# Optimization experiments

Measured on AMD Instinct MI355X. Metric: run time of the kernel, lower is better.

The kernel has to match this reference:

```python
import jax, jax.numpy as jnp
import numpy as np

B, D, N, C = 8192, 128, 64, 256

def setup_inputs() -> dict:
    key = jax.random.key(0)
    ks = jax.random.split(key, 7)
    s1 = 1.0 / np.sqrt(D)
    s2 = 1.0 / np.sqrt(C)
    return {
        "X": jax.random.normal(ks[0], (B, D, N), dtype=jnp.float32),
        "W1": jax.random.normal(ks[1], (D, C), dtype=jnp.float32) * s1,
        "b1": jax.random.normal(ks[2], (C,), dtype=jnp.float32) * s1,
        "W2": jax.random.normal(ks[3], (C, C), dtype=jnp.float32) * s2,
        "b2": jax.random.normal(ks[4], (C,), dtype=jnp.float32) * s2,
        "W3": jax.random.normal(ks[5], (C, 1), dtype=jnp.float32) * s2,
        "b3": jax.random.normal(ks[6], (1,), dtype=jnp.float32) * s2,
    }

def reference(X, W1, b1, W2, b2, W3, b3):
    # X: (B, D, N); each per-node slice X[:, :, i] goes through the shared MLP.
    # Batched over nodes: one GEMM instead of N tiny launches.
    h = jax.nn.relu(jnp.einsum('bdn,dc->bnc', X, W1) + b1)   # (B, N, C)
    h = jax.nn.relu(jnp.einsum('bnc,ce->bne', h, W2) + b2)   # (B, N, C)
    logits = jnp.einsum('bnc,co->bno', h, W3) + b3           # (B, N, 1)
    logits = logits[..., 0]                                   # (B, N)
    zeros = jnp.zeros((X.shape[0], 1), dtype=logits.dtype)    # add_zero=True
    return jnp.concatenate([zeros, logits], axis=1)           # (B, N+1)
```

## Files before the change

kernel.cpp:

```cpp
#include <hip/hip_runtime.h>
#include <hip/hip_bf16.h>

typedef unsigned short u16;
typedef unsigned int   u32;
typedef __attribute__((ext_vector_type(8))) short bf16x8;
typedef __attribute__((ext_vector_type(4))) float f32x4;

#define NB 8192

__device__ __forceinline__ u32 pack2bf(float a, float b) {
    __hip_bfloat162 h = __float22bfloat162_rn(make_float2(a, b));
    return *reinterpret_cast<u32*>(&h);
}

__device__ __forceinline__ u16 f2bf(float x) {
    u32 u = __float_as_uint(x);
    u32 r = u + 0x7FFFu + ((u >> 16) & 1u);
    return (u16)(r >> 16);
}

__global__ __launch_bounds__(256) void prep_weights(
    const float* __restrict__ W1, const float* __restrict__ W2,
    u16* __restrict__ w1fr, u16* __restrict__ w2fr)
{
    int tid = blockIdx.x * 256 + threadIdx.x;
    if (tid < 32768) {
        const int f = tid >> 9, r = tid & 511, l = r >> 3, j = r & 7;
        const int wv = f >> 4, mt = (f >> 2) & 3, ks = f & 3;
        const int c = 64 * wv + 16 * mt + (l & 15);
        const int d = 32 * ks + 8 * (l >> 4) + j;
        w1fr[tid] = f2bf(W1[d * 256 + c]);
    } else {
        const int t2 = tid - 32768;
        if (t2 < 65536) {
            const int f = t2 >> 9, r = t2 & 511, l = r >> 3, j = r & 7;
            const int wv = f >> 5, et = (f >> 3) & 3, ks = f & 7;
            const int e = 64 * wv + 16 * et + (l & 15);
            const int c = 32 * ks + 8 * (l >> 4) + j;
            w2fr[t2] = f2bf(W2[c * 256 + e]);
        }
    }
}

__global__ __launch_bounds__(256, 4) void fused_mlp(
    const float* __restrict__ X,
    const float* __restrict__ b1, const float* __restrict__ b2,
    const float* __restrict__ W3, const float* __restrict__ b3,
    const u16* __restrict__ w1fr, const u16* __restrict__ w2fr,
    float* __restrict__ out)
{
    __shared__ __align__(16) u16 smem[64 * 256];
    u16* xt   = smem;
    u16* h1s  = smem;
    __shared__ float partl[4][64];

    const int tid = threadIdx.x;
    const int w   = tid >> 6;
    const int l   = tid & 63;
    const int lc  = l & 15;
    const int lk  = l >> 4;
    const int b   = blockIdx.x;
    const float* Xb = X + (size_t)b * 8192;

    const u16* w1b = w1fr + w * 8192  + l * 8;
    const u16* w2b = w2fr + w * 16384 + l * 8;

    #pragma unroll
    for (int it = 0; it < 4; ++it) {
        const int dc = w + 4 * it, d0 = dc << 3;
        float v[8];
        #pragma unroll
        for (int j = 0; j < 8; ++j) v[j] = Xb[(d0 + j) * 64 + l];
        u32 pk[4];
        #pragma unroll
        for (int j = 0; j < 4; ++j) pk[j] = pack2bf(v[2 * j], v[2 * j + 1]);
        *(uint4*)(xt + l * 128 + ((dc ^ lc) << 3)) = make_uint4(pk[0], pk[1], pk[2], pk[3]);
    }

    bf16x8 afrN[4];
    #pragma unroll
    for (int mt = 0; mt < 4; ++mt)
        afrN[mt] = *(const bf16x8*)(w1b + mt * 2048);
    __syncthreads();

    f32x4 acc[4][4];
    #pragma unroll
    for (int mt = 0; mt < 4; ++mt) {
        const float4 bq = *(const float4*)(b1 + 64 * w + 16 * mt + 4 * lk);
        #pragma unroll
        for (int nt = 0; nt < 4; ++nt)
            acc[mt][nt] = (f32x4){bq.x, bq.y, bq.z, bq.w};
    }

    #pragma unroll
    for (int ks = 0; ks < 4; ++ks) {
        bf16x8 afr[4], bfr[4];
        #pragma unroll
        for (int mt = 0; mt < 4; ++mt) afr[mt] = afrN[mt];
        if (ks < 3) {
            #pragma unroll
            for (int mt = 0; mt < 4; ++mt)
                afrN[mt] = *(const bf16x8*)(w1b + (mt * 4 + ks + 1) * 512);
        }
        #pragma unroll
        for (int nt = 0; nt < 4; ++nt)
            bfr[nt] = *(const bf16x8*)(xt + (16 * nt + lc) * 128 + (((4 * ks + lk) ^ lc) << 3));
        #pragma unroll
        for (int mt = 0; mt < 4; ++mt)
            #pragma unroll
            for (int nt = 0; nt < 4; ++nt)
                acc[mt][nt] = __builtin_amdgcn_mfma_f32_16x16x32_bf16(afr[mt], bfr[nt], acc[mt][nt], 0, 0, 0);
    }
    __syncthreads();

    #pragma unroll
    for (int mt = 0; mt < 4; ++mt) {
        const int c0 = 64 * w + 16 * mt + 4 * lk;
        #pragma unroll
        for (int nt = 0; nt < 4; ++nt) {
            const int n = 16 * nt + lc;
            float x0 = fmaxf(acc[mt][nt][0], 0.f);
            float x1 = fmaxf(acc[mt][nt][1], 0.f);
            float x2 = fmaxf(acc[mt][nt][2], 0.f);
            float x3 = fmaxf(acc[mt][nt][3], 0.f);
            const int chunk = (c0 >> 3) ^ lc;
            *(uint2*)(h1s + n * 256 + (chunk << 3) + (c0 & 7)) =
                make_uint2(pack2bf(x0, x1), pack2bf(x2, x3));
        }
    }

    bf16x8 bfrN[4];
    #pragma unroll
    for (int nt = 0; nt < 4; ++nt)
        bfrN[nt] = *(const bf16x8*)(w2b + nt * 4096);
    __syncthreads();

    f32x4 acc2[4][4];
    float w3v[4];
    #pragma unroll
    for (int nt = 0; nt < 4; ++nt) {
        const int e = 64 * w + 16 * nt + lc;
        const float bv = b2[e];
        w3v[nt] = W3[e];
        #pragma unroll
        for (int mt = 0; mt < 4; ++mt)
            acc2[mt][nt] = (f32x4){bv, bv, bv, bv};
    }

    #pragma unroll
    for (int ks = 0; ks < 8; ++ks) {
        bf16x8 afr[4], bfr[4];
        #pragma unroll
        for (int nt = 0; nt < 4; ++nt) bfr[nt] = bfrN[nt];
        if (ks < 7) {
            #pragma unroll
            for (int nt = 0; nt < 4; ++nt)
                bfrN[nt] = *(const bf16x8*)(w2b + (nt * 8 + ks + 1) * 512);
        }
        #pragma unroll
        for (int mt = 0; mt < 4; ++mt)
            afr[mt] = *(const bf16x8*)(h1s + (16 * mt + lc) * 256 + (((4 * ks + lk) ^ lc) << 3));
        #pragma unroll
        for (int mt = 0; mt < 4; ++mt)
            #pragma unroll
            for (int nt = 0; nt < 4; ++nt)
                acc2[mt][nt] = __builtin_amdgcn_mfma_f32_16x16x32_bf16(afr[mt], bfr[nt], acc2[mt][nt], 0, 0, 0);
    }

    #pragma unroll
    for (int mt = 0; mt < 4; ++mt) {
        #pragma unroll
        for (int j = 0; j < 4; ++j) {
            float s = 0.f;
            #pragma unroll
            for (int nt = 0; nt < 4; ++nt)
                s += fmaxf(acc2[mt][nt][j], 0.f) * w3v[nt];
            s += __shfl_xor(s, 1);
            s += __shfl_xor(s, 2);
            s += __shfl_xor(s, 4);
            s += __shfl_xor(s, 8);
            if (lc == 0) partl[w][16 * mt + 4 * lk + j] = s;
        }
    }
    __syncthreads();

    if (tid < 64) {
        float s = partl[0][tid] + partl[1][tid] + partl[2][tid] + partl[3][tid] + b3[0];
        out[(size_t)b * 65 + 1 + tid] = s;
    } else if (tid == 64) {
        out[(size_t)b * 65] = 0.f;
    }
}

extern "C" void kernel_launch(void* const* d_in, const int* in_sizes, int n_in,
                              void* d_out, int out_size, void* d_ws, size_t ws_size,
                              hipStream_t stream) {
    const float* X  = (const float*)d_in[0];
    const float* W1 = (const float*)d_in[1];
    const float* b1 = (const float*)d_in[2];
    const float* W2 = (const float*)d_in[3];
    const float* b2 = (const float*)d_in[4];
    const float* W3 = (const float*)d_in[5];
    const float* b3 = (const float*)d_in[6];
    float* out = (float*)d_out;

    u16* w1fr = (u16*)d_ws;
    u16* w2fr = w1fr + 32768;

    const int B = in_sizes[0] / (128 * 64);

    prep_weights<<<384, 256, 0, stream>>>(W1, W2, w1fr, w2fr);
    fused_mlp<<<B, 256, 0, stream>>>(X, b1, b2, W3, b3, w1fr, w2fr, out);
}
```

Before: 137.0 us.

## Split work per wave by node rows to drop block barriers and cross-wave reduction

```diff
diff --git a/kernel.cpp b/kernel.cpp
--- a/kernel.cpp
+++ b/kernel.cpp
@@ -26,16 +26,16 @@
     int tid = blockIdx.x * 256 + threadIdx.x;
     if (tid < 32768) {
         const int f = tid >> 9, r = tid & 511, l = r >> 3, j = r & 7;
-        const int wv = f >> 4, mt = (f >> 2) & 3, ks = f & 3;
-        const int c = 64 * wv + 16 * mt + (l & 15);
+        const int m = f >> 2, ks = f & 3;
+        const int c = 16 * m + (l & 15);
         const int d = 32 * ks + 8 * (l >> 4) + j;
         w1fr[tid] = f2bf(W1[d * 256 + c]);
     } else {
         const int t2 = tid - 32768;
         if (t2 < 65536) {
             const int f = t2 >> 9, r = t2 & 511, l = r >> 3, j = r & 7;
-            const int wv = f >> 5, et = (f >> 3) & 3, ks = f & 7;
-            const int e = 64 * wv + 16 * et + (l & 15);
+            const int t = f >> 3, ks = f & 7;
+            const int e = 16 * t + (l & 15);
             const int c = 32 * ks + 8 * (l >> 4) + j;
             w2fr[t2] = f2bf(W2[c * 256 + e]);
         }
@@ -49,11 +49,7 @@
     const u16* __restrict__ w1fr, const u16* __restrict__ w2fr,
     float* __restrict__ out)
 {
-    __shared__ __align__(16) u16 smem[64 * 256];
-    u16* xt   = smem;
-    u16* h1s  = smem;
-    __shared__ float partl[4][64];
-
+    __shared__ __align__(16) u16 arena[4 * 4096];
     const int tid = threadIdx.x;
     const int w   = tid >> 6;
     const int l   = tid & 63;
@@ -62,134 +58,91 @@
     const int b   = blockIdx.x;
     const float* Xb = X + (size_t)b * 8192;
 
-    const u16* w1b = w1fr + w * 8192  + l * 8;
-    const u16* w2b = w2fr + w * 16384 + l * 8;
+    u16* const W = arena + w * 4096;
 
     #pragma unroll
-    for (int it = 0; it < 4; ++it) {
-        const int dc = w + 4 * it, d0 = dc << 3;
+    for (int i = 0; i < 4; ++i) {
+        const int dc = lk + 4 * i, d0 = dc << 3;
         float v[8];
         #pragma unroll
-        for (int j = 0; j < 8; ++j) v[j] = Xb[(d0 + j) * 64 + l];
+        for (int j = 0; j < 8; ++j)
+            v[j] = Xb[(d0 + j) * 64 + 16 * w + lc];
         u32 pk[4];
         #pragma unroll
         for (int j = 0; j < 4; ++j) pk[j] = pack2bf(v[2 * j], v[2 * j + 1]);
-        *(uint4*)(xt + l * 128 + ((dc ^ lc) << 3)) = make_uint4(pk[0], pk[1], pk[2], pk[3]);
+        *(uint4*)(W + lc * 128 + (((dc ^ lc) & 15) << 3)) = make_uint4(pk[0], pk[1], pk[2], pk[3]);
     }
 
-    bf16x8 afrN[4];
+    f32x4 acc[16];
     #pragma unroll
-    for (int mt = 0; mt < 4; ++mt)
-        afrN[mt] = *(const bf16x8*)(w1b + mt * 2048);
-    __syncthreads();
+    for (int m = 0; m < 16; ++m) acc[m] = (f32x4){0.f, 0.f, 0.f, 0.f};
 
-    f32x4 acc[4][4];
     #pragma unroll
-    for (int mt = 0; mt < 4; ++mt) {
-        const float4 bq = *(const float4*)(b1 + 64 * w + 16 * mt + 4 * lk);
+    for (int ks = 0; ks < 4; ++ks) {
+        const bf16x8 bfr = *(const bf16x8*)(W + lc * 128 + ((((4 * ks + lk) ^ lc) & 15) << 3));
         #pragma unroll
-        for (int nt = 0; nt < 4; ++nt)
-            acc[mt][nt] = (f32x4){bq.x, bq.y, bq.z, bq.w};
+        for (int m = 0; m < 16; ++m) {
+            const bf16x8 afr = *(const bf16x8*)(w1fr + (m * 4 + ks) * 512 + l * 8);
+            acc[m] = __builtin_amdgcn_mfma_f32_16x16x32_bf16(afr, bfr, acc[m], 0, 0, 0);
+        }
     }
 
     #pragma unroll
-    for (int ks = 0; ks < 4; ++ks) {
-        bf16x8 afr[4], bfr[4];
-        #pragma unroll
-        for (int mt = 0; mt < 4; ++mt) afr[mt] = afrN[mt];
-        if (ks < 3) {
-            #pragma unroll
-            for (int mt = 0; mt < 4; ++mt)
-                afrN[mt] = *(const bf16x8*)(w1b + (mt * 4 + ks + 1) * 512);
-        }
-        #pragma unroll
-        for (int nt = 0; nt < 4; ++nt)
-            bfr[nt] = *(const bf16x8*)(xt + (16 * nt + lc) * 128 + (((4 * ks + lk) ^ lc) << 3));
-        #pragma unroll
-        for (int mt = 0; mt < 4; ++mt)
-            #pragma unroll
-            for (int nt = 0; nt < 4; ++nt)
-                acc[mt][nt] = __builtin_amdgcn_mfma_f32_16x16x32_bf16(afr[mt], bfr[nt], acc[mt][nt], 0, 0, 0);
+    for (int m = 0; m < 16; ++m) {
+        const int c0 = 16 * m + 4 * lk;
+        const float4 bq = *(const float4*)(b1 + c0);
+        float x0 = fmaxf(acc[m][0] + bq.x, 0.f);
+        float x1 = fmaxf(acc[m][1] + bq.y, 0.f);
+        float x2 = fmaxf(acc[m][2] + bq.z, 0.f);
+        float x3 = fmaxf(acc[m][3] + bq.w, 0.f);
+        const int slot = ((c0 >> 3) ^ lc) & 31;
+        *(uint2*)(W + lc * 256 + (slot << 3) + (c0 & 7)) =
+            make_uint2(pack2bf(x0, x1), pack2bf(x2, x3));
     }
-    __syncthreads();
+
+    f32x4 acc2[16];
+    #pragma unroll
+    for (int t = 0; t < 16; ++t) acc2[t] = (f32x4){0.f, 0.f, 0.f, 0.f};
 
     #pragma unroll
-    for (int mt = 0; mt < 4; ++mt) {
-        const int c0 = 64 * w + 16 * mt + 4 * lk;
+    for (int ks = 0; ks < 8; ++ks) {
+        const bf16x8 afr = *(const bf16x8*)(W + lc * 256 + ((((4 * ks + lk) ^ lc) & 31) << 3));
         #pragma unroll
-        for (int nt = 0; nt < 4; ++nt) {
-            const int n = 16 * nt + lc;
-            float x0 = fmaxf(acc[mt][nt][0], 0.f);
-            float x1 = fmaxf(acc[mt][nt][1], 0.f);
-            float x2 = fmaxf(acc[mt][nt][2], 0.f);
-            float x3 = fmaxf(acc[mt][nt][3], 0.f);
-            const int chunk = (c0 >> 3) ^ lc;
-            *(uint2*)(h1s + n * 256 + (chunk << 3) + (c0 & 7)) =
-                make_uint2(pack2bf(x0, x1), pack2bf(x2, x3));
+        for (int t = 0; t < 16; ++t) {
+            const bf16x8 bfr = *(const bf16x8*)(w2fr + (t * 8 + ks) * 512 + l * 8);
+            acc2[t] = __builtin_amdgcn_mfma_f32_16x16x32_bf16(afr, bfr, acc2[t], 0, 0, 0);
         }
     }
 
-    bf16x8 bfrN[4];
+    float s0 = 0.f, s1 = 0.f, s2 = 0.f, s3 = 0.f;
     #pragma unroll
-    for (int nt = 0; nt < 4; ++nt)
-        bfrN[nt] = *(const bf16x8*)(w2b + nt * 4096);
-    __syncthreads();
-
-    f32x4 acc2[4][4];
-    float w3v[4];
+    for (int t = 0; t < 16; ++t) {
+        const int e = 16 * t + lc;
+        const float bv = b2[e];
+        const float wv = W3[e];
+        s0 += fmaxf(acc2[t][0] + bv, 0.f) * wv;
+        s1 += fmaxf(acc2[t][1] + bv, 0.f) * wv;
+        s2 += fmaxf(acc2[t][2] + bv, 0.f) * wv;
+        s3 += fmaxf(acc2[t][3] + bv, 0.f) * wv;
+    }
+    float sr[4] = {s0, s1, s2, s3};
     #pragma unroll
-    for (int nt = 0; nt < 4; ++nt) {
-        const int e = 64 * w + 16 * nt + lc;
-        const float bv = b2[e];
-        w3v[nt] = W3[e];
+    for (int r = 0; r < 4; ++r) {
+        float s = sr[r];
+        s += __shfl_xor(s, 1);
+        s += __shfl_xor(s, 2);
+        s += __shfl_xor(s, 4);
+        s += __shfl_xor(s, 8);
+        sr[r] = s;
+    }
+    if (lc == 0) {
+        const float b3v = b3[0];
+        const int n0 = 16 * w + 4 * lk;
         #pragma unroll
-        for (int mt = 0; mt < 4; ++mt)
-            acc2[mt][nt] = (f32x4){bv, bv, bv, bv};
+        for (int r = 0; r < 4; ++r)
+            out[(size_t)b * 65 + 1 + n0 + r] = sr[r] + b3v;
     }
-
-    #pragma unroll
-    for (int ks = 0; ks < 8; ++ks) {
-        bf16x8 afr[4], bfr[4];
-        #pragma unroll
-        for (int nt = 0; nt < 4; ++nt) bfr[nt] = bfrN[nt];
-        if (ks < 7) {
-            #pragma unroll
-            for (int nt = 0; nt < 4; ++nt)
-                bfrN[nt] = *(const bf16x8*)(w2b + (nt * 8 + ks + 1) * 512);
-        }
-        #pragma unroll
-        for (int mt = 0; mt < 4; ++mt)
-            afr[mt] = *(const bf16x8*)(h1s + (16 * mt + lc) * 256 + (((4 * ks + lk) ^ lc) << 3));
-        #pragma unroll
-        for (int mt = 0; mt < 4; ++mt)
-            #pragma unroll
-            for (int nt = 0; nt < 4; ++nt)
-                acc2[mt][nt] = __builtin_amdgcn_mfma_f32_16x16x32_bf16(afr[mt], bfr[nt], acc2[mt][nt], 0, 0, 0);
-    }
-
-    #pragma unroll
-    for (int mt = 0; mt < 4; ++mt) {
-        #pragma unroll
-        for (int j = 0; j < 4; ++j) {
-            float s = 0.f;
-            #pragma unroll
-            for (int nt = 0; nt < 4; ++nt)
-                s += fmaxf(acc2[mt][nt][j], 0.f) * w3v[nt];
-            s += __shfl_xor(s, 1);
-            s += __shfl_xor(s, 2);
-            s += __shfl_xor(s, 4);
-            s += __shfl_xor(s, 8);
-            if (lc == 0) partl[w][16 * mt + 4 * lk + j] = s;
-        }
-    }
-    __syncthreads();
-
-    if (tid < 64) {
-        float s = partl[0][tid] + partl[1][tid] + partl[2][tid] + partl[3][tid] + b3[0];
-        out[(size_t)b * 65 + 1 + tid] = s;
-    } else if (tid == 64) {
-        out[(size_t)b * 65] = 0.f;
-    }
+    if (tid == 0) out[(size_t)b * 65] = 0.f;
 }
 
 extern "C" void kernel_launch(void* const* d_in, const int* in_sizes, int n_in,
```

Measured after the change: 399.0 us (median of 2 runs). 191% more time.
